# Kernel tuning notes

Measured on AMD Instinct MI355X. Metric: run time of the kernel, lower is better.

The kernel has to match this reference:

```python
import jax, jax.numpy as jnp
import numpy as np

N_NODES = 20000
N_EDGES = 320000
IN_CH = 64
GROWTH = 64
N_BLOCKS = 3


def setup_inputs() -> dict:
    key = jax.random.key(0)
    ks = jax.random.split(key, 8)
    x = jax.random.normal(ks[0], (N_NODES, IN_CH), dtype=jnp.float32)
    edge_index = jax.random.randint(ks[1], (2, N_EDGES), 0, N_NODES, dtype=jnp.int32)
    params = {}
    for i in range(N_BLOCKS):
        fan_in = 2 * (IN_CH + i * GROWTH)
        scale = 1.0 / np.sqrt(fan_in)
        params[f"W{i}"] = jax.random.normal(ks[2 + i], (fan_in, GROWTH), dtype=jnp.float32) * scale
        params[f"b{i}"] = jnp.zeros((GROWTH,), dtype=jnp.float32)
    return {"x": x, "W0": params["W0"], "b0": params["b0"],
            "W1": params["W1"], "b1": params["b1"],
            "W2": params["W2"], "b2": params["b2"],
            "edge_index": edge_index}


def _edge_conv(x, src, dst, W, b, n_nodes):
    # PyG EdgeConv: message = nn(cat[x_i, x_j - x_i]), aggr='max'
    xi = x[dst]                                   # target features  [E, C]
    xj = x[src]                                   # source features  [E, C]
    feat = jnp.concatenate([xi, xj - xi], axis=-1)  # [E, 2C]
    msg = jax.nn.relu(feat @ W + b)               # [E, growth]
    agg = jax.ops.segment_max(msg, dst, num_segments=n_nodes)  # [N, growth]
    # nodes with no incoming edges -> identity (-inf) replaced by 0 (PyG scatter-max behavior)
    return jnp.where(jnp.isfinite(agg), agg, 0.0)


def reference(x, W0, b0, W1, b1, W2, b2, edge_index):
    src, dst = edge_index[0], edge_index[1]
    n = x.shape[0]
    for W, b in ((W0, b0), (W1, b1), (W2, b2)):
        out = _edge_conv(x, src, dst, W, b, n)
        x = jnp.concatenate([x, out], axis=-1)    # dense connectivity
    # [N, growth*(n_blocks+1)] -> [N, growth, n_blocks+1] (row-major, same as torch)
    x = x.reshape(n, GROWTH, N_BLOCKS + 1)
    return jnp.max(x, axis=-1)
```

## Files before the change

kernel.cpp:

```cpp
#include <hip/hip_runtime.h>
#include <hip/hip_bf16.h>

#define NN 20000
#define NE 320000
#define XSTB 256
#define CAP 96

typedef __attribute__((ext_vector_type(8))) short short8v;
typedef __attribute__((ext_vector_type(4))) float float4v;

struct bh4 { __hip_bfloat16 a, b, c, d; };

#define WT_OFF0 0
#define WT_OFF1 (128 * 64)
#define WT_OFF2 (128 * 64 + 128 * 128)
#define WT_TOT  (128 * 64 + 128 * 128 + 128 * 192)

__global__ __launch_bounds__(256) void prep_kernel(const float* __restrict__ x,
                                                   const float* __restrict__ W0,
                                                   const float* __restrict__ W1,
                                                   const float* __restrict__ W2,
                                                   __hip_bfloat16* __restrict__ xcatb,
                                                   __hip_bfloat16* __restrict__ Wt,
                                                   int* __restrict__ cursor) {
    int blk = blockIdx.x, tid = threadIdx.x;
    if (blk < 1250) {
        int i = blk * 256 + tid;
        int n = i >> 4, c4 = (i & 15) << 2;
        float4 v = *(const float4*)(x + (size_t)n * 64 + c4);
        bh4 o = {__float2bfloat16(v.x), __float2bfloat16(v.y),
                 __float2bfloat16(v.z), __float2bfloat16(v.w)};
        *(bh4*)(xcatb + (size_t)n * XSTB + c4) = o;
    } else if (blk < 1250 + 192) {
        int e = (blk - 1250) * 256 + tid;
        const float* W;
        int K, off;
        if (e < WT_OFF1) { W = W0; K = 64;  off = WT_OFF0; }
        else if (e < WT_OFF2) { W = W1; K = 128; off = WT_OFF1; }
        else { W = W2; K = 192; off = WT_OFF2; }
        int el = e - off;
        int j = el / K, k = el - j * K;
        float w;
        if (j < 64) w = W[(size_t)k * 64 + j] - W[(size_t)(K + k) * 64 + j];
        else        w = W[(size_t)(K + k) * 64 + (j - 64)];
        Wt[(size_t)off + (size_t)j * K + k] = __float2bfloat16(w);
    } else {
        int idx = (blk - 1442) * 256 + tid;
        if (idx < NN) cursor[idx] = 0;
    }
}

__global__ __launch_bounds__(256) void fillb_kernel(const int* __restrict__ src,
                                                    const int* __restrict__ dst,
                                                    int* __restrict__ cursor,
                                                    int* __restrict__ elist) {
    int i = blockIdx.x * 256 + threadIdx.x;
    if (i < NE) {
        int d = dst[i];
        int pos = atomicAdd(cursor + d, 1);
        if (pos < CAP) elist[(size_t)d * CAP + pos] = src[i];
    }
}

template <int C>
__global__ __launch_bounds__(256) void gemm3_kernel(const __hip_bfloat16* __restrict__ xcatb,
                                                    const __hip_bfloat16* __restrict__ Wt,
                                                    float* __restrict__ Pa,
                                                    __hip_bfloat16* __restrict__ Pbb) {
    int tid = threadIdx.x;
    int wid = blockIdx.x * 4 + (tid >> 6);
    int lane = tid & 63;
    int panel = wid >> 1;
    int half = wid & 1;
    int m = lane & 15, g = lane >> 4;
    const __hip_bfloat16* aptr = xcatb + (size_t)(panel * 16 + m) * XSTB + g * 8;
    const __hip_bfloat16* bptr = Wt + (size_t)(half * 64 + m) * C + g * 8;

    float4v acc[4] = {{0.f, 0.f, 0.f, 0.f}, {0.f, 0.f, 0.f, 0.f},
                      {0.f, 0.f, 0.f, 0.f}, {0.f, 0.f, 0.f, 0.f}};
#pragma unroll
    for (int k0 = 0; k0 < C; k0 += 32) {
        short8v a = *(const short8v*)(aptr + k0);
#pragma unroll
        for (int t = 0; t < 4; ++t) {
            short8v b = *(const short8v*)(bptr + (size_t)t * 16 * C + k0);
            acc[t] = __builtin_amdgcn_mfma_f32_16x16x32_bf16(a, b, acc[t], 0, 0, 0);
        }
    }
    int r0 = panel * 16;
    if (half == 0) {
#pragma unroll
        for (int t = 0; t < 4; ++t)
#pragma unroll
            for (int r = 0; r < 4; ++r)
                Pa[(size_t)(r0 + g * 4 + r) * 64 + t * 16 + m] = acc[t][r];
    } else {
#pragma unroll
        for (int t = 0; t < 4; ++t)
#pragma unroll
            for (int r = 0; r < 4; ++r)
                Pbb[(size_t)(r0 + g * 4 + r) * 64 + t * 16 + m] = __float2bfloat16(acc[t][r]);
    }
}

__device__ __forceinline__ float bucket_max(const int* __restrict__ el, int c, int lane,
                                            const __hip_bfloat16* __restrict__ Pbb) {
    float mx = -INFINITY;
    int i = 0;
    for (; i + 4 <= c; i += 4) {
        int s0 = el[i], s1 = el[i + 1], s2 = el[i + 2], s3 = el[i + 3];
        float v0 = __bfloat162float(Pbb[(size_t)s0 * 64 + lane]);
        float v1 = __bfloat162float(Pbb[(size_t)s1 * 64 + lane]);
        float v2 = __bfloat162float(Pbb[(size_t)s2 * 64 + lane]);
        float v3 = __bfloat162float(Pbb[(size_t)s3 * 64 + lane]);
        mx = fmaxf(mx, fmaxf(fmaxf(v0, v1), fmaxf(v2, v3)));
    }
    for (; i < c; ++i) {
        int s = el[i];
        mx = fmaxf(mx, __bfloat162float(Pbb[(size_t)s * 64 + lane]));
    }
    return mx;
}

__global__ __launch_bounds__(256) void agg_kernel(const float* __restrict__ Pa,
                                                  const __hip_bfloat16* __restrict__ Pbb,
                                                  const float* __restrict__ b,
                                                  const int* __restrict__ cnt,
                                                  const int* __restrict__ elist,
                                                  __hip_bfloat16* __restrict__ xcatb,
                                                  int outoff) {
    int wid = (int)((blockIdx.x * 256 + threadIdx.x) >> 6);
    int lane = threadIdx.x & 63;
    int c = cnt[wid];
    if (c > CAP) c = CAP;
    float mx = bucket_max(elist + (size_t)wid * CAP, c, lane, Pbb);
    float v = fmaxf(Pa[(size_t)wid * 64 + lane] + b[lane] + mx, 0.f);
    xcatb[(size_t)wid * XSTB + outoff + lane] = __float2bfloat16(v);
}

__global__ __launch_bounds__(256) void aggf_kernel(const float* __restrict__ Pa,
                                                   const __hip_bfloat16* __restrict__ Pbb,
                                                   const float* __restrict__ b,
                                                   const int* __restrict__ cnt,
                                                   const int* __restrict__ elist,
                                                   const __hip_bfloat16* __restrict__ xcatb,
                                                   float* __restrict__ out) {
    __shared__ float sm[4][64];
    int w = threadIdx.x >> 6, lane = threadIdx.x & 63;
    int wid = blockIdx.x * 4 + w;
    int c = cnt[wid];
    if (c > CAP) c = CAP;
    float mx = bucket_max(elist + (size_t)wid * CAP, c, lane, Pbb);
    float v = fmaxf(Pa[(size_t)wid * 64 + lane] + b[lane] + mx, 0.f);
    sm[w][lane] = v;
    __syncthreads();
    float m;
    if (lane < 48) {
        bh4 q = *(const bh4*)(xcatb + (size_t)wid * XSTB + (lane << 2));
        float f0 = __bfloat162float(q.a), f1 = __bfloat162float(q.b);
        float f2 = __bfloat162float(q.c), f3 = __bfloat162float(q.d);
        m = fmaxf(fmaxf(f0, f1), fmaxf(f2, f3));
    } else {
        const float* p = &sm[w][(lane - 48) << 2];
        m = fmaxf(fmaxf(p[0], p[1]), fmaxf(p[2], p[3]));
    }
    out[(size_t)wid * 64 + lane] = m;
}

extern "C" void kernel_launch(void* const* d_in, const int* in_sizes, int n_in,
                              void* d_out, int out_size, void* d_ws, size_t ws_size,
                              hipStream_t stream) {
    const float* x = (const float*)d_in[0];
    const float* W0 = (const float*)d_in[1];
    const float* W1 = (const float*)d_in[3];
    const float* W2 = (const float*)d_in[5];
    const float* bp[3] = {(const float*)d_in[2], (const float*)d_in[4], (const float*)d_in[6]};
    const int* eidx = (const int*)d_in[7];
    const int* esrc = eidx;
    const int* edst = eidx + NE;
    float* out = (float*)d_out;

    char* w = (char*)d_ws;
    __hip_bfloat16* xcatb = (__hip_bfloat16*)w;  w += (size_t)NN * XSTB * 2;
    float* Pa = (float*)w;                       w += (size_t)NN * 64 * 4;
    __hip_bfloat16* Pbb = (__hip_bfloat16*)w;    w += (size_t)NN * 64 * 2;
    __hip_bfloat16* Wt = (__hip_bfloat16*)w;     w += (size_t)WT_TOT * 2;
    int* cursor = (int*)w;                       w += (size_t)NN * 4;
    int* elist = (int*)w;

    prep_kernel<<<1250 + 192 + 79, 256, 0, stream>>>(x, W0, W1, W2, xcatb, Wt, cursor);
    fillb_kernel<<<(NE + 255) / 256, 256, 0, stream>>>(esrc, edst, cursor, elist);

    gemm3_kernel<64><<<625, 256, 0, stream>>>(xcatb, Wt + WT_OFF0, Pa, Pbb);
    agg_kernel<<<(NN + 3) / 4, 256, 0, stream>>>(Pa, Pbb, bp[0], cursor, elist, xcatb, 64);
    gemm3_kernel<128><<<625, 256, 0, stream>>>(xcatb, Wt + WT_OFF1, Pa, Pbb);
    agg_kernel<<<(NN + 3) / 4, 256, 0, stream>>>(Pa, Pbb, bp[1], cursor, elist, xcatb, 128);
    gemm3_kernel<192><<<625, 256, 0, stream>>>(xcatb, Wt + WT_OFF2, Pa, Pbb);
    aggf_kernel<<<(NN + 3) / 4, 256, 0, stream>>>(Pa, Pbb, bp[2], cursor, elist, xcatb, out);
}
```

Measured before the change: 108.7 us.

## Fuse aggregation with next layer GEMM using shared-memory tile and ping-pong buffers

Merges each aggregation kernel with the following block's GEMM. A 256-thread block aggregates 16 nodes into a shared-memory tile, writes them to xcatb, then two waves run the MFMA GEMM, reading the new columns from LDS. Ping-pong Pa/Pbb buffers avoid read-after-write races across blocks. This removes two launches and a global round trip for the new features, but half the waves sit idle during the GEMM phase and the aggregation grid shrinks from 5000 to 1250 blocks.

```diff
diff --git a/kernel.cpp b/kernel.cpp
--- a/kernel.cpp
+++ b/kernel.cpp
@@ -62,28 +62,25 @@
     }
 }
 
-template <int C>
-__global__ __launch_bounds__(256) void gemm3_kernel(const __hip_bfloat16* __restrict__ xcatb,
+__global__ __launch_bounds__(256) void gemm0_kernel(const __hip_bfloat16* __restrict__ xcatb,
                                                     const __hip_bfloat16* __restrict__ Wt,
                                                     float* __restrict__ Pa,
                                                     __hip_bfloat16* __restrict__ Pbb) {
     int tid = threadIdx.x;
     int wid = blockIdx.x * 4 + (tid >> 6);
     int lane = tid & 63;
-    int panel = wid >> 1;
-    int half = wid & 1;
+    int panel = wid >> 1, half = wid & 1;
     int m = lane & 15, g = lane >> 4;
     const __hip_bfloat16* aptr = xcatb + (size_t)(panel * 16 + m) * XSTB + g * 8;
-    const __hip_bfloat16* bptr = Wt + (size_t)(half * 64 + m) * C + g * 8;
-
-    float4v acc[4] = {{0.f, 0.f, 0.f, 0.f}, {0.f, 0.f, 0.f, 0.f},
-                      {0.f, 0.f, 0.f, 0.f}, {0.f, 0.f, 0.f, 0.f}};
-#pragma unroll
-    for (int k0 = 0; k0 < C; k0 += 32) {
+    const __hip_bfloat16* bptr = Wt + (size_t)(half * 64 + m) * 64 + g * 8;
+
+    float4v acc[4] = {{0.f,0.f,0.f,0.f},{0.f,0.f,0.f,0.f},{0.f,0.f,0.f,0.f},{0.f,0.f,0.f,0.f}};
+#pragma unroll
+    for (int k0 = 0; k0 < 64; k0 += 32) {
         short8v a = *(const short8v*)(aptr + k0);
 #pragma unroll
         for (int t = 0; t < 4; ++t) {
-            short8v b = *(const short8v*)(bptr + (size_t)t * 16 * C + k0);
+            short8v b = *(const short8v*)(bptr + (size_t)t * 16 * 64 + k0);
             acc[t] = __builtin_amdgcn_mfma_f32_16x16x32_bf16(a, b, acc[t], 0, 0, 0);
         }
     }
@@ -122,20 +119,67 @@
     return mx;
 }
 
-__global__ __launch_bounds__(256) void agg_kernel(const float* __restrict__ Pa,
-                                                  const __hip_bfloat16* __restrict__ Pbb,
-                                                  const float* __restrict__ b,
-                                                  const int* __restrict__ cnt,
-                                                  const int* __restrict__ elist,
-                                                  __hip_bfloat16* __restrict__ xcatb,
-                                                  int outoff) {
-    int wid = (int)((blockIdx.x * 256 + threadIdx.x) >> 6);
-    int lane = threadIdx.x & 63;
-    int c = cnt[wid];
-    if (c > CAP) c = CAP;
-    float mx = bucket_max(elist + (size_t)wid * CAP, c, lane, Pbb);
-    float v = fmaxf(Pa[(size_t)wid * 64 + lane] + b[lane] + mx, 0.f);
-    xcatb[(size_t)wid * XSTB + outoff + lane] = __float2bfloat16(v);
+template <int C>
+__global__ __launch_bounds__(256) void fused_kernel(const float* __restrict__ PaIn,
+                                                    const __hip_bfloat16* __restrict__ PbbIn,
+                                                    const float* __restrict__ b,
+                                                    const int* __restrict__ cnt,
+                                                    const int* __restrict__ elist,
+                                                    __hip_bfloat16* __restrict__ xcatb,
+                                                    const __hip_bfloat16* __restrict__ Wt,
+                                                    float* __restrict__ PaOut,
+                                                    __hip_bfloat16* __restrict__ PbbOut) {
+    __shared__ __hip_bfloat16 newt[16][72];
+    int tid = threadIdx.x;
+    int w = tid >> 6, lane = tid & 63;
+    int panel = blockIdx.x;
+    int r0 = panel * 16;
+
+#pragma unroll
+    for (int nl = 0; nl < 4; ++nl) {
+        int local = w * 4 + nl;
+        int node = r0 + local;
+        int c = cnt[node];
+        if (c > CAP) c = CAP;
+        float mx = bucket_max(elist + (size_t)node * CAP, c, lane, PbbIn);
+        float v = fmaxf(PaIn[(size_t)node * 64 + lane] + b[lane] + mx, 0.f);
+        __hip_bfloat16 h = __float2bfloat16(v);
+        newt[local][lane] = h;
+        xcatb[(size_t)node * XSTB + (C - 64) + lane] = h;
+    }
+    __syncthreads();
+    if (w >= 2) return;
+
+    int half = w;
+    int m = lane & 15, g = lane >> 4;
+    const __hip_bfloat16* aptr = xcatb + (size_t)(r0 + m) * XSTB + g * 8;
+    const __hip_bfloat16* bptr = Wt + (size_t)(half * 64 + m) * C + g * 8;
+
+    float4v acc[4] = {{0.f,0.f,0.f,0.f},{0.f,0.f,0.f,0.f},{0.f,0.f,0.f,0.f},{0.f,0.f,0.f,0.f}};
+#pragma unroll
+    for (int k0 = 0; k0 < C; k0 += 32) {
+        short8v a;
+        if (k0 < C - 64) a = *(const short8v*)(aptr + k0);
+        else             a = *(const short8v*)(&newt[m][k0 - (C - 64) + g * 8]);
+#pragma unroll
+        for (int t = 0; t < 4; ++t) {
+            short8v bb = *(const short8v*)(bptr + (size_t)t * 16 * C + k0);
+            acc[t] = __builtin_amdgcn_mfma_f32_16x16x32_bf16(a, bb, acc[t], 0, 0, 0);
+        }
+    }
+    if (half == 0) {
+#pragma unroll
+        for (int t = 0; t < 4; ++t)
+#pragma unroll
+            for (int r = 0; r < 4; ++r)
+                PaOut[(size_t)(r0 + g * 4 + r) * 64 + t * 16 + m] = acc[t][r];
+    } else {
+#pragma unroll
+        for (int t = 0; t < 4; ++t)
+#pragma unroll
+            for (int r = 0; r < 4; ++r)
+                PbbOut[(size_t)(r0 + g * 4 + r) * 64 + t * 16 + m] = __float2bfloat16(acc[t][r]);
+    }
 }
 
 __global__ __launch_bounds__(256) void aggf_kernel(const float* __restrict__ Pa,
@@ -182,8 +226,10 @@
 
     char* w = (char*)d_ws;
     __hip_bfloat16* xcatb = (__hip_bfloat16*)w;  w += (size_t)NN * XSTB * 2;
-    float* Pa = (float*)w;                       w += (size_t)NN * 64 * 4;
-    __hip_bfloat16* Pbb = (__hip_bfloat16*)w;    w += (size_t)NN * 64 * 2;
+    float* PaA = (float*)w;                      w += (size_t)NN * 64 * 4;
+    __hip_bfloat16* PbbA = (__hip_bfloat16*)w;   w += (size_t)NN * 64 * 2;
+    float* PaB = (float*)w;                      w += (size_t)NN * 64 * 4;
+    __hip_bfloat16* PbbB = (__hip_bfloat16*)w;   w += (size_t)NN * 64 * 2;
     __hip_bfloat16* Wt = (__hip_bfloat16*)w;     w += (size_t)WT_TOT * 2;
     int* cursor = (int*)w;                       w += (size_t)NN * 4;
     int* elist = (int*)w;
@@ -191,10 +237,10 @@
     prep_kernel<<<1250 + 192 + 79, 256, 0, stream>>>(x, W0, W1, W2, xcatb, Wt, cursor);
     fillb_kernel<<<(NE + 255) / 256, 256, 0, stream>>>(esrc, edst, cursor, elist);
 
-    gemm3_kernel<64><<<625, 256, 0, stream>>>(xcatb, Wt + WT_OFF0, Pa, Pbb);
-    agg_kernel<<<(NN + 3) / 4, 256, 0, stream>>>(Pa, Pbb, bp[0], cursor, elist, xcatb, 64);
-    gemm3_kernel<128><<<625, 256, 0, stream>>>(xcatb, Wt + WT_OFF1, Pa, Pbb);
-    agg_kernel<<<(NN + 3) / 4, 256, 0, stream>>>(Pa, Pbb, bp[1], cursor, elist, xcatb, 128);
-    gemm3_kernel<192><<<625, 256, 0, stream>>>(xcatb, Wt + WT_OFF2, Pa, Pbb);
-    aggf_kernel<<<(NN + 3) / 4, 256, 0, stream>>>(Pa, Pbb, bp[2], cursor, elist, xcatb, out);
-}
+    gemm0_kernel<<<625, 256, 0, stream>>>(xcatb, Wt + WT_OFF0, PaA, PbbA);
+    fused_kernel<128><<<1250, 256, 0, stream>>>(PaA, PbbA, bp[0], cursor, elist, xcatb,
+                                                Wt + WT_OFF1, PaB, PbbB);
+    fused_kernel<192><<<1250, 256, 0, stream>>>(PaB, PbbB, bp[1], cursor, elist, xcatb,
+                                                Wt + WT_OFF2, PaA, PbbA);
+    aggf_kernel<<<(NN + 3) / 4, 256, 0, stream>>>(PaA, PbbA, bp[2], cursor, elist, xcatb, out);
+}
```

Measured after the change: 96.96 us. 10.8% less time.
